# Kernel tuning notes

Hardware: AMD Instinct MI355X
Metric: run time of the kernel (lower is better)

The kernel has to match this reference:

```python
import jax, jax.numpy as jnp
import numpy as np

B, S, DIN, D, H, L, DFF = 256, 100, 64, 256, 8, 6, 1024
DK = D // H
SCALE = float(np.sqrt(DK))

def _pe(s, d):
    pos = np.arange(s)[:, None].astype(np.float32)
    div = np.exp(np.arange(0, d, 2).astype(np.float32) * (-np.log(10000.0) / d))
    pe = np.zeros((s, d), np.float32)
    pe[:, 0::2] = np.sin(pos * div)
    pe[:, 1::2] = np.cos(pos * div)
    return jnp.asarray(pe)

PE = _pe(S, D)  # (S, D) sinusoidal positional encoding

def _ln(x, g, b, eps=1e-5):
    m = jnp.mean(x, -1, keepdims=True)
    v = jnp.mean((x - m) ** 2, -1, keepdims=True)
    return (x - m) * jax.lax.rsqrt(v + eps) * g + b

def setup_inputs() -> dict:
    ks = iter(jax.random.split(jax.random.key(0), 32))
    def w(*shape):
        return jax.random.normal(next(ks), shape, jnp.float32) * 0.02
    z = lambda *s: jnp.zeros(s, jnp.float32)
    o = lambda *s: jnp.ones(s, jnp.float32)
    return {
        'x': jax.random.normal(next(ks), (B, S, DIN), jnp.float32),
        'W_in': w(DIN, D), 'b_in': z(D),
        'Wq': w(L, D, D), 'bq': z(L, D),
        'Wk': w(L, D, D), 'bk': z(L, D),
        'Wv': w(L, D, D), 'bv': z(L, D),
        'Wo': w(L, D, D), 'bo': z(L, D),
        'g1': o(L, D), 'be1': z(L, D),
        'W1': w(L, D, DFF), 'b1': z(L, DFF),
        'W2': w(L, DFF, D), 'b2': z(L, D),
        'g2': o(L, D), 'be2': z(L, D),
        'lnf_g': o(D), 'lnf_b': z(D),
        'Wr1': w(D, 128), 'br1': z(128), 'Wr2': w(128, 3), 'br2': z(3),
        'Wa1': w(D, 128), 'ba1': z(128), 'Wa2': w(128, 64), 'ba2': z(64), 'Wa3': w(64, 1), 'ba3': z(1),
        'Wc1': w(D, 64), 'bc1': z(64), 'Wc2': w(64, 1), 'bc2': z(1),
        'Wv1': w(D, 64), 'bv1': z(64), 'Wv2': w(64, 1), 'bv2': z(1),
    }

def reference(x, W_in, b_in, Wq, bq, Wk, bk, Wv, bv, Wo, bo, g1, be1, W1, b1, W2, b2, g2, be2, lnf_g, lnf_b, Wr1, br1, Wr2, br2, Wa1, ba1, Wa2, ba2, Wa3, ba3, Wc1, bc1, Wc2, bc2, Wv1, bv1, Wv2, bv2):
    h = x @ W_in + b_in + PE  # (B, S, D); dropout is identity in eval mode

    def block(h, p):
        wq, bq_, wk, bk_, wv, bv_, wo, bo_, g1_, be1_, w1, b1_, w2, b2_, g2_, be2_ = p
        q = (h @ wq + bq_).reshape(B, S, H, DK)
        k = (h @ wk + bk_).reshape(B, S, H, DK)
        v = (h @ wv + bv_).reshape(B, S, H, DK)
        s = jnp.einsum('bqhd,bkhd->bhqk', q, k) / SCALE
        a = jax.nn.softmax(s, axis=-1)
        o = jnp.einsum('bhqk,bkhd->bqhd', a, v).reshape(B, S, D)
        h = _ln(h + o @ wo + bo_, g1_, be1_)
        f = jax.nn.relu(h @ w1 + b1_) @ w2 + b2_
        h = _ln(h + f, g2_, be2_)
        return h, None

    h, _ = jax.lax.scan(block, h, (Wq, bq, Wk, bk, Wv, bv, Wo, bo, g1, be1, W1, b1, W2, b2, g2, be2))
    h = _ln(h, lnf_g, lnf_b)
    hf = h[:, -1]  # seq_lengths=None -> last token
    regime = jax.nn.softmax(jax.nn.relu(hf @ Wr1 + br1) @ Wr2 + br2, axis=-1)
    action = jnp.tanh(jax.nn.relu(jax.nn.relu(hf @ Wa1 + ba1) @ Wa2 + ba2) @ Wa3 + ba3)
    confidence = jax.nn.sigmoid(jax.nn.relu(hf @ Wc1 + bc1) @ Wc2 + bc2)
    volatility = jax.nn.relu(jax.nn.relu(hf @ Wv1 + bv1) @ Wv2 + bv2)
    return action, regime, confidence, volatility, hf
```

## Files before the change

kernel.cpp:

```cpp
#include <hip/hip_runtime.h>
#include <hip/hip_bf16.h>

#define BB   256
#define SS   100
#define DIN  64
#define DD   256
#define HH   8
#define LL   6
#define DFF  1024
#define MM   (BB*SS)
#define INV_SCALE 0.17677669529663687f

typedef unsigned short u16;
typedef __attribute__((__ext_vector_type__(8))) __bf16 bf16x8;
typedef __attribute__((__ext_vector_type__(8))) unsigned short u16x8;
typedef __attribute__((__ext_vector_type__(4))) float  f32x4;

__device__ __forceinline__ u16 f2bf(float f) {
    unsigned u = __float_as_uint(f);
    u += 0x7FFFu + ((u >> 16) & 1u);
    return (u16)(u >> 16);
}

#define MFMA16(a,b,c) __builtin_amdgcn_mfma_f32_16x16x32_bf16((a),(b),(c),0,0,0)

#if defined(__has_builtin)
#if __has_builtin(__builtin_amdgcn_global_load_lds)
#define HAVE_GLDS 1
#endif
#endif

#ifdef HAVE_GLDS
typedef __attribute__((address_space(1))) const void gas_void;
typedef __attribute__((address_space(3))) void las_void;
__device__ __forceinline__ void gload16(const u16* g, u16* l) {
    __builtin_amdgcn_global_load_lds((gas_void*)g, (las_void*)l, 16, 0, 0);
}
#else
__device__ __forceinline__ void gload16(const u16* g, u16* l) {
    const int lane = threadIdx.x & 63;
    *(uint4*)((char*)l + lane * 16) = *(const uint4*)g;
}
#endif

__global__ void pe_init_kernel(float* __restrict__ pe) {
    int i = blockIdx.x * blockDim.x + threadIdx.x;
    if (i >= SS * DD) return;
    int s = i >> 8;
    int c = i & 255;
    int ce = c & ~1;
    double div = exp((double)ce * -0.03597789207803197);
    double ang = (double)s * div;
    pe[i] = (float)((c & 1) ? cos(ang) : sin(ang));
}

__global__ void conv_bf16(const float* __restrict__ in, u16* __restrict__ out, int n) {
    int i = blockIdx.x * 256 + threadIdx.x;
    if (i < n) out[i] = f2bf(in[i]);
}

__global__ __launch_bounds__(256)
void transpose_conv(const float* __restrict__ in, u16* __restrict__ out,
                    int K, int N, long outLstride) {
    __shared__ float tile[32][33];
    const int k0 = blockIdx.x * 32, n0 = blockIdx.y * 32, lz = blockIdx.z;
    const int tx = threadIdx.x & 31, ty = threadIdx.x >> 5;
    const float* src = in + (size_t)lz * K * N;
#pragma unroll
    for (int i = 0; i < 4; ++i)
        tile[ty + i*8][tx] = src[(size_t)(k0 + ty + i*8) * N + n0 + tx];
    __syncthreads();
    u16* dst = out + (size_t)lz * outLstride;
#pragma unroll
    for (int i = 0; i < 4; ++i)
        dst[(size_t)(n0 + ty + i*8) * K + k0 + tx] = f2bf(tile[tx][ty + i*8]);
}

__global__ void pack_bias(const float* __restrict__ bq, const float* __restrict__ bk,
                          const float* __restrict__ bv, float* __restrict__ bqkv) {
    int idx = blockIdx.x * 256 + threadIdx.x;
    if (idx >= LL * 768) return;
    int l = idx / 768, c = idx % 768;
    float v = (c < 256) ? bq[l*256 + c] : (c < 512) ? bk[l*256 + c - 256] : bv[l*256 + c - 512];
    bqkv[idx] = v;
}

template<int EPI, bool OF32, bool OBF16>
__global__ __launch_bounds__(256)
void mfma_gemm(const u16* __restrict__ A, const u16* __restrict__ Wt,
               const float* __restrict__ bias, const float* __restrict__ pe,
               float* __restrict__ Cf, u16* __restrict__ Cb,
               int M, int N, int K) {
    __shared__ u16 As[128 * 32];
    __shared__ u16 Bs[128 * 32];
    const int t = threadIdx.x, w = t >> 6, l = t & 63;
    const int bm = blockIdx.x * 128, bn = blockIdx.y * 128;
    const int wr = (w >> 1) * 64, wc = (w & 1) * 64;
    const int lr = l & 15, lk = (l >> 4) * 8, lq = (l >> 4) * 4;
    const int srow = l >> 2, scol = (l & 3) * 8;

    f32x4 acc[4][4] = {};
    const u16* Ag = &A [(size_t)(bm + w * 32 + srow) * K + scol];
    const u16* Bg = &Wt[(size_t)(bn + w * 32 + srow) * K + scol];
    u16* Al = &As[(w * 32) * 32];
    u16* Bl = &Bs[(w * 32) * 32];

    for (int k0 = 0; k0 < K; k0 += 32) {
        gload16(Ag + k0,                  Al);
        gload16(Ag + k0 + (size_t)16 * K, Al + 16 * 32);
        gload16(Bg + k0,                  Bl);
        gload16(Bg + k0 + (size_t)16 * K, Bl + 16 * 32);
        __syncthreads();

        bf16x8 af[4], bfr[4];
#pragma unroll
        for (int m = 0; m < 4; ++m) af[m]  = *(const bf16x8*)&As[(wr + m*16 + lr) * 32 + lk];
#pragma unroll
        for (int n = 0; n < 4; ++n) bfr[n] = *(const bf16x8*)&Bs[(wc + n*16 + lr) * 32 + lk];
#pragma unroll
        for (int m = 0; m < 4; ++m)
#pragma unroll
            for (int n = 0; n < 4; ++n)
                acc[m][n] = MFMA16(af[m], bfr[n], acc[m][n]);
        __syncthreads();
    }

#pragma unroll
    for (int n = 0; n < 4; ++n) {
        const int col = bn + wc + n*16 + lr;
        const float bv = bias[col];
#pragma unroll
        for (int m = 0; m < 4; ++m) {
#pragma unroll
            for (int j = 0; j < 4; ++j) {
                const int row = bm + wr + m*16 + lq + j;
                float v = acc[m][n][j] + bv;
                if (EPI == 1) v = fmaxf(v, 0.f);
                if (EPI == 2) v += pe[(row % SS) * DD + col];
                if (OF32)  Cf[(size_t)row * N + col] = v;
                if (OBF16) Cb[(size_t)row * N + col] = f2bf(v);
            }
        }
    }
}

__global__ __launch_bounds__(256)
void gemm_ln(const u16* __restrict__ A, const u16* __restrict__ Wt,
             const float* __restrict__ bias, const float* __restrict__ g,
             const float* __restrict__ be, float* __restrict__ h,
             u16* __restrict__ hb, int K) {
    __shared__ u16 As[64 * 32];
    __shared__ u16 Bs[256 * 32];
    __shared__ float red[64][4];
    const int t = threadIdx.x, w = t >> 6, l = t & 63;
    const int bm = blockIdx.x * 64;
    const int wr = (w >> 1), wc = (w & 1);
    const int lr = l & 15, lk = (l >> 4) * 8, lq = (l >> 4) * 4;
    const int srow = l >> 2, scol = (l & 3) * 8;

    f32x4 acc[2][8] = {};
    const u16* Ag = &A [(size_t)(bm + w * 16 + srow) * K + scol];
    const u16* Bg = &Wt[(size_t)(w * 64 + srow) * K + scol];
    u16* Al = &As[(w * 16) * 32];
    u16* Bl = &Bs[(w * 64) * 32];

    for (int k0 = 0; k0 < K; k0 += 32) {
        gload16(Ag + k0,                  Al);
        gload16(Bg + k0,                  Bl);
        gload16(Bg + k0 + (size_t)16 * K, Bl + 16 * 32);
        gload16(Bg + k0 + (size_t)32 * K, Bl + 32 * 32);
        gload16(Bg + k0 + (size_t)48 * K, Bl + 48 * 32);
        __syncthreads();

        bf16x8 af[2], bf[8];
#pragma unroll
        for (int mf = 0; mf < 2; ++mf) af[mf] = *(const bf16x8*)&As[(wr*32 + mf*16 + lr) * 32 + lk];
#pragma unroll
        for (int n = 0; n < 8; ++n)    bf[n]  = *(const bf16x8*)&Bs[(wc*128 + n*16 + lr) * 32 + lk];
#pragma unroll
        for (int mf = 0; mf < 2; ++mf)
#pragma unroll
            for (int n = 0; n < 8; ++n)
                acc[mf][n] = MFMA16(af[mf], bf[n], acc[mf][n]);
        __syncthreads();
    }

    float bv[8], gv[8], bev[8];
#pragma unroll
    for (int n = 0; n < 8; ++n) {
        int col = wc*128 + n*16 + lr;
        bv[n] = bias[col]; gv[n] = g[col]; bev[n] = be[col];
    }
#pragma unroll
    for (int mf = 0; mf < 2; ++mf) {
#pragma unroll
        for (int j = 0; j < 4; ++j) {
            const int rloc = wr*32 + mf*16 + lq + j;
            const int row  = bm + rloc;
            float s1 = 0.f, s2 = 0.f;
#pragma unroll
            for (int n = 0; n < 8; ++n) {
                float v = acc[mf][n][j] + bv[n] + h[(size_t)row * DD + wc*128 + n*16 + lr];
                acc[mf][n][j] = v;
                s1 += v; s2 += v * v;
            }
            s1 += __shfl_xor(s1, 1); s2 += __shfl_xor(s2, 1);
            s1 += __shfl_xor(s1, 2); s2 += __shfl_xor(s2, 2);
            s1 += __shfl_xor(s1, 4); s2 += __shfl_xor(s2, 4);
            s1 += __shfl_xor(s1, 8); s2 += __shfl_xor(s2, 8);
            if (lr == 0) { red[rloc][wc*2] = s1; red[rloc][wc*2+1] = s2; }
        }
    }
    __syncthreads();
#pragma unroll
    for (int mf = 0; mf < 2; ++mf) {
#pragma unroll
        for (int j = 0; j < 4; ++j) {
            const int rloc = wr*32 + mf*16 + lq + j;
            const int row  = bm + rloc;
            float s1 = red[rloc][0] + red[rloc][2];
            float s2 = red[rloc][1] + red[rloc][3];
            float mean = s1 * (1.f/DD);
            float var  = s2 * (1.f/DD) - mean*mean;
            float rstd = rsqrtf(var + 1e-5f);
#pragma unroll
            for (int n = 0; n < 8; ++n) {
                int col = wc*128 + n*16 + lr;
                float y = (acc[mf][n][j] - mean) * rstd * gv[n] + bev[n];
                h [(size_t)row * DD + col] = y;
                hb[(size_t)row * DD + col] = f2bf(y);
            }
        }
    }
}

__global__ __launch_bounds__(256)
void attn_mfma(const u16* __restrict__ qkv, u16* __restrict__ ao) {
    const int b = blockIdx.x >> 3, hh = blockIdx.x & 7;
    const int t = threadIdx.x, w = t >> 6, l = t & 63;
    const int lr = l & 15, lk = (l >> 4) * 8, lq = (l >> 4) * 4;
    __shared__ u16 Vt[32 * 136];
    __shared__ u16 Ps[4][32 * 136];
    const size_t rbase = (size_t)b * SS * 768;
    const int qc = hh * 32, kc = 256 + hh * 32, vc = 512 + hh * 32;

    for (int u = t; u < 400; u += 256) {
        int s = u >> 2, dp = (u & 3) * 8;
        u16x8 vv = *(const u16x8*)&qkv[rbase + (size_t)s * 768 + vc + dp];
#pragma unroll
        for (int e = 0; e < 8; ++e) Vt[(dp + e) * 136 + s] = vv[e];
    }
    for (int i = t; i < 32 * 36; i += 256) {
        int d = i / 36, s2 = 100 + i % 36;
        Vt[d * 136 + s2] = 0;
    }

    u16x8 qz = {0,0,0,0,0,0,0,0};
    u16x8 qfr[2];
#pragma unroll
    for (int m = 0; m < 2; ++m) {
        int r = w * 32 + m * 16 + lr;
        qfr[m] = (r < SS) ? *(const u16x8*)&qkv[rbase + (size_t)r * 768 + qc + lk] : qz;
    }

    f32x4 sacc[2][7] = {};
#pragma unroll
    for (int n = 0; n < 7; ++n) {
        int r = n * 16 + lr;
        u16x8 kfr = (r < SS) ? *(const u16x8*)&qkv[rbase + (size_t)r * 768 + kc + lk] : qz;
#pragma unroll
        for (int m = 0; m < 2; ++m)
            sacc[m][n] = MFMA16(*(bf16x8*)&qfr[m], *(bf16x8*)&kfr, sacc[m][n]);
    }

#pragma unroll
    for (int m = 0; m < 2; ++m) {
#pragma unroll
        for (int j = 0; j < 4; ++j) {
            float mx = -1e30f;
#pragma unroll
            for (int n = 0; n < 7; ++n) {
                float s = sacc[m][n][j] * INV_SCALE;
                if (n == 6 && lr >= 4) s = -1e30f;
                sacc[m][n][j] = s;
                mx = fmaxf(mx, s);
            }
            mx = fmaxf(mx, __shfl_xor(mx, 1));
            mx = fmaxf(mx, __shfl_xor(mx, 2));
            mx = fmaxf(mx, __shfl_xor(mx, 4));
            mx = fmaxf(mx, __shfl_xor(mx, 8));
            float sum = 0.f;
#pragma unroll
            for (int n = 0; n < 7; ++n) {
                float p = expf(sacc[m][n][j] - mx);
                if (n == 6 && lr >= 4) p = 0.f;
                sacc[m][n][j] = p;
                sum += p;
            }
            sum += __shfl_xor(sum, 1);
            sum += __shfl_xor(sum, 2);
            sum += __shfl_xor(sum, 4);
            sum += __shfl_xor(sum, 8);
            float inv = 1.f / sum;
#pragma unroll
            for (int n = 0; n < 7; ++n) sacc[m][n][j] *= inv;
        }
    }

    u16* myP = &Ps[w][0];
    for (int i = l; i < 32 * 24; i += 64) {
        int r = i / 24, c2 = 112 + i % 24;
        myP[r * 136 + c2] = 0;
    }
#pragma unroll
    for (int m = 0; m < 2; ++m)
#pragma unroll
        for (int n = 0; n < 7; ++n)
#pragma unroll
            for (int j = 0; j < 4; ++j)
                myP[(m*16 + lq + j) * 136 + n*16 + lr] = f2bf(sacc[m][n][j]);

    __syncthreads();

    f32x4 oacc[2][2] = {};
#pragma unroll
    for (int ks = 0; ks < 4; ++ks) {
        bf16x8 pf[2], vf[2];
#pragma unroll
        for (int m = 0; m < 2; ++m) pf[m] = *(const bf16x8*)&myP[(m*16 + lr) * 136 + ks*32 + lk];
#pragma unroll
        for (int n = 0; n < 2; ++n) vf[n] = *(const bf16x8*)&Vt [(n*16 + lr) * 136 + ks*32 + lk];
#pragma unroll
        for (int m = 0; m < 2; ++m)
#pragma unroll
            for (int n = 0; n < 2; ++n)
                oacc[m][n] = MFMA16(pf[m], vf[n], oacc[m][n]);
    }
#pragma unroll
    for (int m = 0; m < 2; ++m)
#pragma unroll
        for (int j = 0; j < 4; ++j) {
            int s = w*32 + m*16 + lq + j;
            if (s < SS) {
#pragma unroll
                for (int n = 0; n < 2; ++n)
                    ao[((size_t)(b*SS + s)) * DD + hh*32 + n*16 + lr] = f2bf(oacc[m][n][j]);
            }
        }
}

__global__ __launch_bounds__(256)
void add_ln_kernel(const float* __restrict__ h, const float* __restrict__ p,
                   const float* __restrict__ g, const float* __restrict__ be,
                   float* __restrict__ out, u16* __restrict__ outb) {
    const int row = blockIdx.x;
    const int c = threadIdx.x;
    const int idx = row * DD + c;
    float x = h[idx];
    if (p) x += p[idx];

    float s1 = x, s2 = x * x;
#pragma unroll
    for (int o = 32; o > 0; o >>= 1) {
        s1 += __shfl_down(s1, o);
        s2 += __shfl_down(s2, o);
    }
    __shared__ float w1[4], w2[4];
    __shared__ float mean_s, rstd_s;
    const int wid = c >> 6, lane = c & 63;
    if (lane == 0) { w1[wid] = s1; w2[wid] = s2; }
    __syncthreads();
    if (c == 0) {
        float t1 = w1[0] + w1[1] + w1[2] + w1[3];
        float t2 = w2[0] + w2[1] + w2[2] + w2[3];
        float m = t1 * (1.0f / DD);
        float v = t2 * (1.0f / DD) - m * m;
        mean_s = m;
        rstd_s = rsqrtf(v + 1e-5f);
    }
    __syncthreads();
    float y = (x - mean_s) * rstd_s * g[c] + be[c];
    out[idx] = y;
    if (outb) outb[idx] = f2bf(y);
}

__global__ __launch_bounds__(128)
void heads_kernel(const float* __restrict__ h,
                  const float* __restrict__ Wr1, const float* __restrict__ br1,
                  const float* __restrict__ Wr2, const float* __restrict__ br2,
                  const float* __restrict__ Wa1, const float* __restrict__ ba1,
                  const float* __restrict__ Wa2, const float* __restrict__ ba2,
                  const float* __restrict__ Wa3, const float* __restrict__ ba3,
                  const float* __restrict__ Wc1, const float* __restrict__ bc1,
                  const float* __restrict__ Wc2, const float* __restrict__ bc2,
                  const float* __restrict__ Wv1, const float* __restrict__ bv1,
                  const float* __restrict__ Wv2, const float* __restrict__ bv2,
                  float* __restrict__ out) {
    const int b = blockIdx.x, t = threadIdx.x;
    __shared__ float hf[DD];
    __shared__ float t1[128];
    __shared__ float t2[64];
    __shared__ float lg[3];
    const int hbase = (b * SS + (SS - 1)) * DD;
    hf[t]       = h[hbase + t];
    hf[t + 128] = h[hbase + t + 128];
    out[1536 + b * DD + t]       = hf[t];
    out[1536 + b * DD + t + 128] = hf[t + 128];
    __syncthreads();

    {
        float acc = br1[t];
        for (int k2 = 0; k2 < DD; ++k2) acc = fmaf(hf[k2], Wr1[k2 * 128 + t], acc);
        t1[t] = fmaxf(acc, 0.f);
    }
    __syncthreads();
    if (t < 3) {
        float a = br2[t];
        for (int k2 = 0; k2 < 128; ++k2) a = fmaf(t1[k2], Wr2[k2 * 3 + t], a);
        lg[t] = a;
    }
    __syncthreads();
    if (t == 0) {
        float m = fmaxf(lg[0], fmaxf(lg[1], lg[2]));
        float e0 = expf(lg[0] - m), e1 = expf(lg[1] - m), e2 = expf(lg[2] - m);
        float inv = 1.0f / (e0 + e1 + e2);
        out[256 + b * 3 + 0] = e0 * inv;
        out[256 + b * 3 + 1] = e1 * inv;
        out[256 + b * 3 + 2] = e2 * inv;
    }
    {
        float acc = ba1[t];
        for (int k2 = 0; k2 < DD; ++k2) acc = fmaf(hf[k2], Wa1[k2 * 128 + t], acc);
        t1[t] = fmaxf(acc, 0.f);
    }
    __syncthreads();
    if (t < 64) {
        float acc = ba2[t];
        for (int k2 = 0; k2 < 128; ++k2) acc = fmaf(t1[k2], Wa2[k2 * 64 + t], acc);
        t2[t] = fmaxf(acc, 0.f);
    }
    __syncthreads();
    if (t == 0) {
        float acc = ba3[0];
        for (int k2 = 0; k2 < 64; ++k2) acc = fmaf(t2[k2], Wa3[k2], acc);
        out[b] = tanhf(acc);
    }
    __syncthreads();
    if (t < 64) {
        float acc = bc1[t];
        for (int k2 = 0; k2 < DD; ++k2) acc = fmaf(hf[k2], Wc1[k2 * 64 + t], acc);
        t2[t] = fmaxf(acc, 0.f);
    }
    __syncthreads();
    if (t == 0) {
        float acc = bc2[0];
        for (int k2 = 0; k2 < 64; ++k2) acc = fmaf(t2[k2], Wc2[k2], acc);
        out[1024 + b] = 1.0f / (1.0f + expf(-acc));
    }
    __syncthreads();
    if (t < 64) {
        float acc = bv1[t];
        for (int k2 = 0; k2 < DD; ++k2) acc = fmaf(hf[k2], Wv1[k2 * 64 + t], acc);
        t2[t] = fmaxf(acc, 0.f);
    }
    __syncthreads();
    if (t == 0) {
        float acc = bv2[0];
        for (int k2 = 0; k2 < 64; ++k2) acc = fmaf(t2[k2], Wv2[k2], acc);
        out[1280 + b] = fmaxf(acc, 0.f);
    }
}

extern "C" void kernel_launch(void* const* d_in, const int* in_sizes, int n_in,
                              void* d_out, int out_size, void* d_ws, size_t ws_size,
                              hipStream_t stream) {
    const float* x    = (const float*)d_in[0];
    const float* W_in = (const float*)d_in[1];
    const float* b_in = (const float*)d_in[2];
    const float* Wq   = (const float*)d_in[3];
    const float* bq   = (const float*)d_in[4];
    const float* Wk   = (const float*)d_in[5];
    const float* bk   = (const float*)d_in[6];
    const float* Wv   = (const float*)d_in[7];
    const float* bv   = (const float*)d_in[8];
    const float* Wo   = (const float*)d_in[9];
    const float* bo   = (const float*)d_in[10];
    const float* g1   = (const float*)d_in[11];
    const float* be1  = (const float*)d_in[12];
    const float* W1   = (const float*)d_in[13];
    const float* b1   = (const float*)d_in[14];
    const float* W2   = (const float*)d_in[15];
    const float* b2   = (const float*)d_in[16];
    const float* g2   = (const float*)d_in[17];
    const float* be2  = (const float*)d_in[18];
    const float* lnf_g = (const float*)d_in[19];
    const float* lnf_b = (const float*)d_in[20];
    const float* Wr1  = (const float*)d_in[21];
    const float* br1  = (const float*)d_in[22];
    const float* Wr2  = (const float*)d_in[23];
    const float* br2  = (const float*)d_in[24];
    const float* Wa1  = (const float*)d_in[25];
    const float* ba1  = (const float*)d_in[26];
    const float* Wa2  = (const float*)d_in[27];
    const float* ba2  = (const float*)d_in[28];
    const float* Wa3  = (const float*)d_in[29];
    const float* ba3  = (const float*)d_in[30];
    const float* Wc1  = (const float*)d_in[31];
    const float* bc1  = (const float*)d_in[32];
    const float* Wc2  = (const float*)d_in[33];
    const float* bc2  = (const float*)d_in[34];
    const float* Wv1  = (const float*)d_in[35];
    const float* bv1  = (const float*)d_in[36];
    const float* Wv2  = (const float*)d_in[37];
    const float* bv2  = (const float*)d_in[38];
    float* out = (float*)d_out;

    char* w8 = (char*)d_ws;
    float* pe   = (float*)w8;  w8 += (size_t)SS * DD * 4;
    float* h    = (float*)w8;  w8 += (size_t)MM * DD * 4;
    float* tmp  = (float*)w8;  w8 += (size_t)MM * DD * 4;
    u16*   hb   = (u16*)w8;    w8 += (size_t)MM * DD * 2;
    u16*   xb   = (u16*)w8;    w8 += (size_t)MM * DIN * 2;
    u16*   qkvb = (u16*)w8;    w8 += (size_t)MM * 768 * 2;
    u16*   ao   = (u16*)w8;    w8 += (size_t)MM * DD * 2;
    u16*   ffn1b= (u16*)w8;    w8 += (size_t)MM * DFF * 2;
    u16*   WinT = (u16*)w8;    w8 += (size_t)DIN * DD * 2;
    u16*   WqkvT= (u16*)w8;    w8 += (size_t)LL * 768 * DD * 2;
    u16*   WoT  = (u16*)w8;    w8 += (size_t)LL * DD * DD * 2;
    u16*   W1T  = (u16*)w8;    w8 += (size_t)LL * DFF * DD * 2;
    u16*   W2T  = (u16*)w8;    w8 += (size_t)LL * DD * DFF * 2;
    float* bqkv = (float*)w8;  w8 += (size_t)LL * 768 * 4;
    (void)tmp;

    pe_init_kernel<<<(SS * DD + 255) / 256, 256, 0, stream>>>(pe);
    conv_bf16<<<(MM * DIN + 255) / 256, 256, 0, stream>>>(x, xb, MM * DIN);
    transpose_conv<<<dim3(DIN/32, DD/32, 1), 256, 0, stream>>>(W_in, WinT, DIN, DD, (long)DIN * DD);
    transpose_conv<<<dim3(8, 8, 6),  256, 0, stream>>>(Wq, WqkvT,             DD, DD, 768L * DD);
    transpose_conv<<<dim3(8, 8, 6),  256, 0, stream>>>(Wk, WqkvT + DD*DD,     DD, DD, 768L * DD);
    transpose_conv<<<dim3(8, 8, 6),  256, 0, stream>>>(Wv, WqkvT + 2*DD*DD,   DD, DD, 768L * DD);
    transpose_conv<<<dim3(8, 8, 6),  256, 0, stream>>>(Wo, WoT, DD, DD, (long)DD * DD);
    transpose_conv<<<dim3(8, 32, 6), 256, 0, stream>>>(W1, W1T, DD, DFF, (long)DD * DFF);
    transpose_conv<<<dim3(32, 8, 6), 256, 0, stream>>>(W2, W2T, DFF, DD, (long)DD * DFF);
    pack_bias<<<(LL * 768 + 255) / 256, 256, 0, stream>>>(bq, bk, bv, bqkv);

    mfma_gemm<2, true, true><<<dim3(MM/128, DD/128), 256, 0, stream>>>(
        xb, WinT, b_in, pe, h, hb, MM, DD, DIN);

    for (int l = 0; l < LL; ++l) {
        mfma_gemm<0, false, true><<<dim3(MM/128, 768/128), 256, 0, stream>>>(
            hb, WqkvT + (size_t)l*768*DD, bqkv + l*768, nullptr, nullptr, qkvb, MM, 768, DD);
        attn_mfma<<<BB * HH, 256, 0, stream>>>(qkvb, ao);
        gemm_ln<<<MM/64, 256, 0, stream>>>(
            ao, WoT + (size_t)l*DD*DD, bo + l*DD, g1 + l*DD, be1 + l*DD, h, hb, DD);
        mfma_gemm<1, false, true><<<dim3(MM/128, DFF/128), 256, 0, stream>>>(
            hb, W1T + (size_t)l*DFF*DD, b1 + l*DFF, nullptr, nullptr, ffn1b, MM, DFF, DD);
        gemm_ln<<<MM/64, 256, 0, stream>>>(
            ffn1b, W2T + (size_t)l*DD*DFF, b2 + l*DD, g2 + l*DD, be2 + l*DD, h, hb, DFF);
    }

    add_ln_kernel<<<MM, DD, 0, stream>>>(h, nullptr, lnf_g, lnf_b, h, nullptr);

    heads_kernel<<<BB, 128, 0, stream>>>(h,
        Wr1, br1, Wr2, br2,
        Wa1, ba1, Wa2, ba2, Wa3, ba3,
        Wc1, bc1, Wc2, bc2,
        Wv1, bv1, Wv2, bv2,
        out);
}
```

Before: 965.0 us.

## Load GEMM fragments directly from global with register prefetch; restrict final LN to last token

The GEMM and GEMM+LayerNorm kernels stop staging tiles through LDS with barriers. Each lane now loads its MFMA fragments straight from global memory and prefetches the next k-step into registers. The final LayerNorm runs only on the last token of each sequence instead of every row, and the first layers of the four output heads are packed into a single bf16 MFMA GEMM. Reading fragments from global gives up the sharing of tiles between waves that LDS provided, so global and L2 traffic rise, and the head outputs now pass through bf16 rounding.

```diff
diff --git a/kernel.cpp b/kernel.cpp
--- a/kernel.cpp
+++ b/kernel.cpp
@@ -24,25 +24,6 @@
 
 #define MFMA16(a,b,c) __builtin_amdgcn_mfma_f32_16x16x32_bf16((a),(b),(c),0,0,0)
 
-#if defined(__has_builtin)
-#if __has_builtin(__builtin_amdgcn_global_load_lds)
-#define HAVE_GLDS 1
-#endif
-#endif
-
-#ifdef HAVE_GLDS
-typedef __attribute__((address_space(1))) const void gas_void;
-typedef __attribute__((address_space(3))) void las_void;
-__device__ __forceinline__ void gload16(const u16* g, u16* l) {
-    __builtin_amdgcn_global_load_lds((gas_void*)g, (las_void*)l, 16, 0, 0);
-}
-#else
-__device__ __forceinline__ void gload16(const u16* g, u16* l) {
-    const int lane = threadIdx.x & 63;
-    *(uint4*)((char*)l + lane * 16) = *(const uint4*)g;
-}
-#endif
-
 __global__ void pe_init_kernel(float* __restrict__ pe) {
     int i = blockIdx.x * blockDim.x + threadIdx.x;
     if (i >= SS * DD) return;
@@ -85,44 +66,63 @@
     bqkv[idx] = v;
 }
 
+__global__ void pack_wh1(const float* __restrict__ Wr1, const float* __restrict__ Wa1,
+                         const float* __restrict__ Wc1, const float* __restrict__ Wv1,
+                         const float* __restrict__ br1, const float* __restrict__ ba1,
+                         const float* __restrict__ bc1, const float* __restrict__ bv1,
+                         u16* __restrict__ Wh1T, float* __restrict__ bh1) {
+    int i = blockIdx.x * 256 + threadIdx.x;
+    if (i < 384 * 256) {
+        int n = i >> 8, k = i & 255;
+        float v = (n < 128) ? Wr1[k*128 + n]
+                : (n < 256) ? Wa1[k*128 + (n-128)]
+                : (n < 320) ? Wc1[k*64  + (n-256)]
+                            : Wv1[k*64  + (n-320)];
+        Wh1T[(size_t)n * 256 + k] = f2bf(v);
+    }
+    if (i < 384) {
+        float v = (i < 128) ? br1[i] : (i < 256) ? ba1[i-128]
+                : (i < 320) ? bc1[i-256] : bv1[i-320];
+        bh1[i] = v;
+    }
+}
+
 template<int EPI, bool OF32, bool OBF16>
 __global__ __launch_bounds__(256)
-void mfma_gemm(const u16* __restrict__ A, const u16* __restrict__ Wt,
-               const float* __restrict__ bias, const float* __restrict__ pe,
-               float* __restrict__ Cf, u16* __restrict__ Cb,
-               int M, int N, int K) {
-    __shared__ u16 As[128 * 32];
-    __shared__ u16 Bs[128 * 32];
+void mfma_gemm_d(const u16* __restrict__ A, const u16* __restrict__ Wt,
+                 const float* __restrict__ bias, const float* __restrict__ pe,
+                 float* __restrict__ Cf, u16* __restrict__ Cb,
+                 int M, int N, int K) {
     const int t = threadIdx.x, w = t >> 6, l = t & 63;
     const int bm = blockIdx.x * 128, bn = blockIdx.y * 128;
     const int wr = (w >> 1) * 64, wc = (w & 1) * 64;
     const int lr = l & 15, lk = (l >> 4) * 8, lq = (l >> 4) * 4;
-    const int srow = l >> 2, scol = (l & 3) * 8;
 
     f32x4 acc[4][4] = {};
-    const u16* Ag = &A [(size_t)(bm + w * 32 + srow) * K + scol];
-    const u16* Bg = &Wt[(size_t)(bn + w * 32 + srow) * K + scol];
-    u16* Al = &As[(w * 32) * 32];
-    u16* Bl = &Bs[(w * 32) * 32];
+    const u16* Ab = A  + (size_t)(bm + wr + lr) * K + lk;
+    const u16* Bb = Wt + (size_t)(bn + wc + lr) * K + lk;
+
+    bf16x8 afc[4], bfc[4], afn[4], bfn[4];
+#pragma unroll
+    for (int m = 0; m < 4; ++m) afc[m] = *(const bf16x8*)(Ab + (size_t)m*16*K);
+#pragma unroll
+    for (int n = 0; n < 4; ++n) bfc[n] = *(const bf16x8*)(Bb + (size_t)n*16*K);
 
     for (int k0 = 0; k0 < K; k0 += 32) {
-        gload16(Ag + k0,                  Al);
-        gload16(Ag + k0 + (size_t)16 * K, Al + 16 * 32);
-        gload16(Bg + k0,                  Bl);
-        gload16(Bg + k0 + (size_t)16 * K, Bl + 16 * 32);
-        __syncthreads();
-
-        bf16x8 af[4], bfr[4];
-#pragma unroll
-        for (int m = 0; m < 4; ++m) af[m]  = *(const bf16x8*)&As[(wr + m*16 + lr) * 32 + lk];
-#pragma unroll
-        for (int n = 0; n < 4; ++n) bfr[n] = *(const bf16x8*)&Bs[(wc + n*16 + lr) * 32 + lk];
+        const int kp = (k0 + 32 < K) ? k0 + 32 : k0;
+#pragma unroll
+        for (int m = 0; m < 4; ++m) afn[m] = *(const bf16x8*)(Ab + (size_t)m*16*K + kp);
+#pragma unroll
+        for (int n = 0; n < 4; ++n) bfn[n] = *(const bf16x8*)(Bb + (size_t)n*16*K + kp);
 #pragma unroll
         for (int m = 0; m < 4; ++m)
 #pragma unroll
             for (int n = 0; n < 4; ++n)
-                acc[m][n] = MFMA16(af[m], bfr[n], acc[m][n]);
-        __syncthreads();
+                acc[m][n] = MFMA16(afc[m], bfc[n], acc[m][n]);
+#pragma unroll
+        for (int m = 0; m < 4; ++m) afc[m] = afn[m];
+#pragma unroll
+        for (int n = 0; n < 4; ++n) bfc[n] = bfn[n];
     }
 
 #pragma unroll
@@ -145,44 +145,41 @@
 }
 
 __global__ __launch_bounds__(256)
-void gemm_ln(const u16* __restrict__ A, const u16* __restrict__ Wt,
-             const float* __restrict__ bias, const float* __restrict__ g,
-             const float* __restrict__ be, float* __restrict__ h,
-             u16* __restrict__ hb, int K) {
-    __shared__ u16 As[64 * 32];
-    __shared__ u16 Bs[256 * 32];
+void gemm_ln_d(const u16* __restrict__ A, const u16* __restrict__ Wt,
+               const float* __restrict__ bias, const float* __restrict__ g,
+               const float* __restrict__ be, float* __restrict__ h,
+               u16* __restrict__ hb, int K) {
     __shared__ float red[64][4];
     const int t = threadIdx.x, w = t >> 6, l = t & 63;
     const int bm = blockIdx.x * 64;
     const int wr = (w >> 1), wc = (w & 1);
     const int lr = l & 15, lk = (l >> 4) * 8, lq = (l >> 4) * 4;
-    const int srow = l >> 2, scol = (l & 3) * 8;
 
     f32x4 acc[2][8] = {};
-    const u16* Ag = &A [(size_t)(bm + w * 16 + srow) * K + scol];
-    const u16* Bg = &Wt[(size_t)(w * 64 + srow) * K + scol];
-    u16* Al = &As[(w * 16) * 32];
-    u16* Bl = &Bs[(w * 64) * 32];
+    const u16* Ab = A  + (size_t)(bm + wr*32 + lr) * K + lk;
+    const u16* Bb = Wt + (size_t)(wc*128 + lr) * K + lk;
+
+    bf16x8 afc[2], bfc[8], afn[2], bfn[8];
+#pragma unroll
+    for (int m = 0; m < 2; ++m) afc[m] = *(const bf16x8*)(Ab + (size_t)m*16*K);
+#pragma unroll
+    for (int n = 0; n < 8; ++n) bfc[n] = *(const bf16x8*)(Bb + (size_t)n*16*K);
 
     for (int k0 = 0; k0 < K; k0 += 32) {
-        gload16(Ag + k0,                  Al);
-        gload16(Bg + k0,                  Bl);
-        gload16(Bg + k0 + (size_t)16 * K, Bl + 16 * 32);
-        gload16(Bg + k0 + (size_t)32 * K, Bl + 32 * 32);
-        gload16(Bg + k0 + (size_t)48 * K, Bl + 48 * 32);
-        __syncthreads();
-
-        bf16x8 af[2], bf[8];
-#pragma unroll
-        for (int mf = 0; mf < 2; ++mf) af[mf] = *(const bf16x8*)&As[(wr*32 + mf*16 + lr) * 32 + lk];
-#pragma unroll
-        for (int n = 0; n < 8; ++n)    bf[n]  = *(const bf16x8*)&Bs[(wc*128 + n*16 + lr) * 32 + lk];
-#pragma unroll
-        for (int mf = 0; mf < 2; ++mf)
+        const int kp = (k0 + 32 < K) ? k0 + 32 : k0;
+#pragma unroll
+        for (int m = 0; m < 2; ++m) afn[m] = *(const bf16x8*)(Ab + (size_t)m*16*K + kp);
+#pragma unroll
+        for (int n = 0; n < 8; ++n) bfn[n] = *(const bf16x8*)(Bb + (size_t)n*16*K + kp);
+#pragma unroll
+        for (int m = 0; m < 2; ++m)
 #pragma unroll
             for (int n = 0; n < 8; ++n)
-                acc[mf][n] = MFMA16(af[mf], bf[n], acc[mf][n]);
-        __syncthreads();
+                acc[m][n] = MFMA16(afc[m], bfc[n], acc[m][n]);
+#pragma unroll
+        for (int m = 0; m < 2; ++m) afc[m] = afn[m];
+#pragma unroll
+        for (int n = 0; n < 8; ++n) bfc[n] = bfn[n];
     }
 
     float bv[8], gv[8], bev[8];
@@ -350,14 +347,13 @@
 }
 
 __global__ __launch_bounds__(256)
-void add_ln_kernel(const float* __restrict__ h, const float* __restrict__ p,
-                   const float* __restrict__ g, const float* __restrict__ be,
-                   float* __restrict__ out, u16* __restrict__ outb) {
-    const int row = blockIdx.x;
+void lastrow_ln(const float* __restrict__ h, const float* __restrict__ g,
+                const float* __restrict__ be, float* __restrict__ out,
+                u16* __restrict__ hfb) {
+    const int b = blockIdx.x;
     const int c = threadIdx.x;
-    const int idx = row * DD + c;
-    float x = h[idx];
-    if (p) x += p[idx];
+    const float* row = h + (size_t)(b * SS + SS - 1) * DD;
+    float x = row[c];
 
     float s1 = x, s2 = x * x;
 #pragma unroll
@@ -380,44 +376,42 @@
     }
     __syncthreads();
     float y = (x - mean_s) * rstd_s * g[c] + be[c];
-    out[idx] = y;
-    if (outb) outb[idx] = f2bf(y);
-}
-
-__global__ __launch_bounds__(128)
-void heads_kernel(const float* __restrict__ h,
-                  const float* __restrict__ Wr1, const float* __restrict__ br1,
-                  const float* __restrict__ Wr2, const float* __restrict__ br2,
-                  const float* __restrict__ Wa1, const float* __restrict__ ba1,
-                  const float* __restrict__ Wa2, const float* __restrict__ ba2,
-                  const float* __restrict__ Wa3, const float* __restrict__ ba3,
-                  const float* __restrict__ Wc1, const float* __restrict__ bc1,
-                  const float* __restrict__ Wc2, const float* __restrict__ bc2,
-                  const float* __restrict__ Wv1, const float* __restrict__ bv1,
-                  const float* __restrict__ Wv2, const float* __restrict__ bv2,
-                  float* __restrict__ out) {
+    out[1536 + b * DD + c] = y;
+    hfb[b * DD + c] = f2bf(y);
+}
+
+__global__ __launch_bounds__(256)
+void heads2_kernel(const float* __restrict__ t1f,
+                   const float* __restrict__ Wr2, const float* __restrict__ br2,
+                   const float* __restrict__ Wa2, const float* __restrict__ ba2,
+                   const float* __restrict__ Wa3, const float* __restrict__ ba3,
+                   const float* __restrict__ Wc2, const float* __restrict__ bc2,
+                   const float* __restrict__ Wv2, const float* __restrict__ bv2,
+                   float* __restrict__ out) {
     const int b = blockIdx.x, t = threadIdx.x;
-    __shared__ float hf[DD];
-    __shared__ float t1[128];
-    __shared__ float t2[64];
+    __shared__ float t1[384];
+    __shared__ float a2[64];
     __shared__ float lg[3];
-    const int hbase = (b * SS + (SS - 1)) * DD;
-    hf[t]       = h[hbase + t];
-    hf[t + 128] = h[hbase + t + 128];
-    out[1536 + b * DD + t]       = hf[t];
-    out[1536 + b * DD + t + 128] = hf[t + 128];
-    __syncthreads();
-
-    {
-        float acc = br1[t];
-        for (int k2 = 0; k2 < DD; ++k2) acc = fmaf(hf[k2], Wr1[k2 * 128 + t], acc);
-        t1[t] = fmaxf(acc, 0.f);
-    }
-    __syncthreads();
-    if (t < 3) {
-        float a = br2[t];
-        for (int k2 = 0; k2 < 128; ++k2) a = fmaf(t1[k2], Wr2[k2 * 3 + t], a);
-        lg[t] = a;
+    for (int i = t; i < 384; i += 256) t1[i] = t1f[(size_t)b * 384 + i];
+    __syncthreads();
+
+    if (t < 64) {
+        float acc = ba2[t];
+        for (int k = 0; k < 128; ++k) acc = fmaf(t1[128 + k], Wa2[k * 64 + t], acc);
+        a2[t] = fmaxf(acc, 0.f);
+    } else if (t == 64) {
+        float acc = bc2[0];
+        for (int k = 0; k < 64; ++k) acc = fmaf(t1[256 + k], Wc2[k], acc);
+        out[1024 + b] = 1.0f / (1.0f + expf(-acc));
+    } else if (t == 65) {
+        float acc = bv2[0];
+        for (int k = 0; k < 64; ++k) acc = fmaf(t1[320 + k], Wv2[k], acc);
+        out[1280 + b] = fmaxf(acc, 0.f);
+    } else if (t >= 66 && t < 69) {
+        int r = t - 66;
+        float acc = br2[r];
+        for (int k = 0; k < 128; ++k) acc = fmaf(t1[k], Wr2[k * 3 + r], acc);
+        lg[r] = acc;
     }
     __syncthreads();
     if (t == 0) {
@@ -428,46 +422,15 @@
         out[256 + b * 3 + 1] = e1 * inv;
         out[256 + b * 3 + 2] = e2 * inv;
     }
-    {
-        float acc = ba1[t];
-        for (int k2 = 0; k2 < DD; ++k2) acc = fmaf(hf[k2], Wa1[k2 * 128 + t], acc);
-        t1[t] = fmaxf(acc, 0.f);
-    }
-    __syncthreads();
     if (t < 64) {
-        float acc = ba2[t];
-        for (int k2 = 0; k2 < 128; ++k2) acc = fmaf(t1[k2], Wa2[k2 * 64 + t], acc);
-        t2[t] = fmaxf(acc, 0.f);
-    }
-    __syncthreads();
-    if (t == 0) {
-        float acc = ba3[0];
-        for (int k2 = 0; k2 < 64; ++k2) acc = fmaf(t2[k2], Wa3[k2], acc);
-        out[b] = tanhf(acc);
-    }
-    __syncthreads();
-    if (t < 64) {
-        float acc = bc1[t];
-        for (int k2 = 0; k2 < DD; ++k2) acc = fmaf(hf[k2], Wc1[k2 * 64 + t], acc);
-        t2[t] = fmaxf(acc, 0.f);
-    }
-    __syncthreads();
-    if (t == 0) {
-        float acc = bc2[0];
-        for (int k2 = 0; k2 < 64; ++k2) acc = fmaf(t2[k2], Wc2[k2], acc);
-        out[1024 + b] = 1.0f / (1.0f + expf(-acc));
-    }
-    __syncthreads();
-    if (t < 64) {
-        float acc = bv1[t];
-        for (int k2 = 0; k2 < DD; ++k2) acc = fmaf(hf[k2], Wv1[k2 * 64 + t], acc);
-        t2[t] = fmaxf(acc, 0.f);
-    }
-    __syncthreads();
-    if (t == 0) {
-        float acc = bv2[0];
-        for (int k2 = 0; k2 < 64; ++k2) acc = fmaf(t2[k2], Wv2[k2], acc);
-        out[1280 + b] = fmaxf(acc, 0.f);
+        float p = a2[t] * Wa3[t];
+        p += __shfl_xor(p, 1);
+        p += __shfl_xor(p, 2);
+        p += __shfl_xor(p, 4);
+        p += __shfl_xor(p, 8);
+        p += __shfl_xor(p, 16);
+        p += __shfl_xor(p, 32);
+        if (t == 0) out[b] = tanhf(p + ba3[0]);
     }
 }
 
@@ -516,21 +479,23 @@
     float* out = (float*)d_out;
 
     char* w8 = (char*)d_ws;
-    float* pe   = (float*)w8;  w8 += (size_t)SS * DD * 4;
-    float* h    = (float*)w8;  w8 += (size_t)MM * DD * 4;
-    float* tmp  = (float*)w8;  w8 += (size_t)MM * DD * 4;
-    u16*   hb   = (u16*)w8;    w8 += (size_t)MM * DD * 2;
-    u16*   xb   = (u16*)w8;    w8 += (size_t)MM * DIN * 2;
-    u16*   qkvb = (u16*)w8;    w8 += (size_t)MM * 768 * 2;
-    u16*   ao   = (u16*)w8;    w8 += (size_t)MM * DD * 2;
-    u16*   ffn1b= (u16*)w8;    w8 += (size_t)MM * DFF * 2;
-    u16*   WinT = (u16*)w8;    w8 += (size_t)DIN * DD * 2;
-    u16*   WqkvT= (u16*)w8;    w8 += (size_t)LL * 768 * DD * 2;
-    u16*   WoT  = (u16*)w8;    w8 += (size_t)LL * DD * DD * 2;
-    u16*   W1T  = (u16*)w8;    w8 += (size_t)LL * DFF * DD * 2;
-    u16*   W2T  = (u16*)w8;    w8 += (size_t)LL * DD * DFF * 2;
-    float* bqkv = (float*)w8;  w8 += (size_t)LL * 768 * 4;
-    (void)tmp;
+    float* pe    = (float*)w8;  w8 += (size_t)SS * DD * 4;
+    float* h     = (float*)w8;  w8 += (size_t)MM * DD * 4;
+    u16*   hb    = (u16*)w8;    w8 += (size_t)MM * DD * 2;
+    u16*   xb    = (u16*)w8;    w8 += (size_t)MM * DIN * 2;
+    u16*   qkvb  = (u16*)w8;    w8 += (size_t)MM * 768 * 2;
+    u16*   ao    = (u16*)w8;    w8 += (size_t)MM * DD * 2;
+    u16*   ffn1b = (u16*)w8;    w8 += (size_t)MM * DFF * 2;
+    u16*   WinT  = (u16*)w8;    w8 += (size_t)DIN * DD * 2;
+    u16*   WqkvT = (u16*)w8;    w8 += (size_t)LL * 768 * DD * 2;
+    u16*   WoT   = (u16*)w8;    w8 += (size_t)LL * DD * DD * 2;
+    u16*   W1T   = (u16*)w8;    w8 += (size_t)LL * DFF * DD * 2;
+    u16*   W2T   = (u16*)w8;    w8 += (size_t)LL * DD * DFF * 2;
+    float* bqkv  = (float*)w8;  w8 += (size_t)LL * 768 * 4;
+    u16*   Wh1T  = (u16*)w8;    w8 += (size_t)384 * 256 * 2;
+    float* bh1   = (float*)w8;  w8 += (size_t)384 * 4;
+    u16*   hfb   = (u16*)w8;    w8 += (size_t)BB * DD * 2;
+    float* t1f   = (float*)w8;  w8 += (size_t)BB * 384 * 4;
 
     pe_init_kernel<<<(SS * DD + 255) / 256, 256, 0, stream>>>(pe);
     conv_bf16<<<(MM * DIN + 255) / 256, 256, 0, stream>>>(x, xb, MM * DIN);
@@ -542,28 +507,28 @@
     transpose_conv<<<dim3(8, 32, 6), 256, 0, stream>>>(W1, W1T, DD, DFF, (long)DD * DFF);
     transpose_conv<<<dim3(32, 8, 6), 256, 0, stream>>>(W2, W2T, DFF, DD, (long)DD * DFF);
     pack_bias<<<(LL * 768 + 255) / 256, 256, 0, stream>>>(bq, bk, bv, bqkv);
-
-    mfma_gemm<2, true, true><<<dim3(MM/128, DD/128), 256, 0, stream>>>(
+    pack_wh1<<<384, 256, 0, stream>>>(Wr1, Wa1, Wc1, Wv1, br1, ba1, bc1, bv1, Wh1T, bh1);
+
+    mfma_gemm_d<2, true, true><<<dim3(MM/128, DD/128), 256, 0, stream>>>(
         xb, WinT, b_in, pe, h, hb, MM, DD, DIN);
 
     for (int l = 0; l < LL; ++l) {
-        mfma_gemm<0, false, true><<<dim3(MM/128, 768/128), 256, 0, stream>>>(
+        mfma_gemm_d<0, false, true><<<dim3(MM/128, 768/128), 256, 0, stream>>>(
             hb, WqkvT + (size_t)l*768*DD, bqkv + l*768, nullptr, nullptr, qkvb, MM, 768, DD);
         attn_mfma<<<BB * HH, 256, 0, stream>>>(qkvb, ao);
-        gemm_ln<<<MM/64, 256, 0, stream>>>(
+        gemm_ln_d<<<MM/64, 256, 0, stream>>>(
             ao, WoT + (size_t)l*DD*DD, bo + l*DD, g1 + l*DD, be1 + l*DD, h, hb, DD);
-        mfma_gemm<1, false, true><<<dim3(MM/128, DFF/128), 256, 0, stream>>>(
+        mfma_gemm_d<1, false, true><<<dim3(MM/128, DFF/128), 256, 0, stream>>>(
             hb, W1T + (size_t)l*DFF*DD, b1 + l*DFF, nullptr, nullptr, ffn1b, MM, DFF, DD);
-        gemm_ln<<<MM/64, 256, 0, stream>>>(
+        gemm_ln_d<<<MM/64, 256, 0, stream>>>(
             ffn1b, W2T + (size_t)l*DD*DFF, b2 + l*DD, g2 + l*DD, be2 + l*DD, h, hb, DFF);
     }
 
-    add_ln_kernel<<<MM, DD, 0, stream>>>(h, nullptr, lnf_g, lnf_b, h, nullptr);
-
-    heads_kernel<<<BB, 128, 0, stream>>>(h,
-        Wr1, br1, Wr2, br2,
-        Wa1, ba1, Wa2, ba2, Wa3, ba3,
-        Wc1, bc1, Wc2, bc2,
-        Wv1, bv1, Wv2, bv2,
-        out);
-}
+    lastrow_ln<<<BB, 256, 0, stream>>>(h, lnf_g, lnf_b, out, hfb);
+
+    mfma_gemm_d<1, true, false><<<dim3(2, 3), 256, 0, stream>>>(
+        hfb, Wh1T, bh1, nullptr, t1f, nullptr, 256, 384, 256);
+
+    heads2_kernel<<<BB, 256, 0, stream>>>(t1f,
+        Wr2, br2, Wa2, ba2, Wa3, ba3, Wc2, bc2, Wv2, bv2, out);
+}
```

New measurement: 1.601 ms. 65.9% more time.
